# Performance work log

Hardware: AMD Instinct MI355X
Metric: run time of the kernel (lower is better)

## Reference

```python
import jax, jax.numpy as jnp
import numpy as np
from jax import lax

DIM = 128
DEPTH = 2
OUT_DIM = 256
DIM_HEAD = 64
HEADS = 8
WS = 16
INNER = DIM_HEAD * HEADS
EPS = 1e-5
SCALE = DIM_HEAD ** (-0.5)


def setup_inputs() -> dict:
    key = jax.random.key(0)
    ks = jax.random.split(key, 20)
    s = 0.02
    L = DEPTH
    inp = {
        "x": jax.random.normal(ks[0], (1, DIM, 256, 256), dtype=jnp.float32),
        "ln1_g": jnp.ones((L, DIM), dtype=jnp.float32),
        "ln1_b": jnp.zeros((L, DIM), dtype=jnp.float32),
        "wq": jax.random.normal(ks[1], (L, INNER, DIM), dtype=jnp.float32) * s,
        "wkv": jax.random.normal(ks[2], (L, 2 * INNER, DIM), dtype=jnp.float32) * s,
        "wo": jax.random.normal(ks[3], (L, DIM, INNER), dtype=jnp.float32) * s,
        "bo": jnp.zeros((L, DIM), dtype=jnp.float32),
        "ln2_g": jnp.ones((L, DIM), dtype=jnp.float32),
        "ln2_b": jnp.zeros((L, DIM), dtype=jnp.float32),
        "w_in": jax.random.normal(ks[4], (L, DIM, DIM), dtype=jnp.float32) * s,
        "b_in": jnp.zeros((L, DIM), dtype=jnp.float32),
        "w_c3": jax.random.normal(ks[5], (L, OUT_DIM, DIM, 3, 3), dtype=jnp.float32) * s,
        "b_c3": jnp.zeros((L, OUT_DIM), dtype=jnp.float32),
        "w_c1": jax.random.normal(ks[6], (L, DIM, OUT_DIM), dtype=jnp.float32) * s,
        "b_c1": jnp.zeros((L, DIM), dtype=jnp.float32),
        "w_outer": jax.random.normal(ks[7], (DIM, DIM), dtype=jnp.float32) * s,
        "b_outer": jnp.zeros((DIM,), dtype=jnp.float32),
    }
    return inp


def _layernorm(x, g, b):
    # channel-wise (dim=1) norm; note torch code uses (std + eps), not sqrt(var + eps)
    mean = jnp.mean(x, axis=1, keepdims=True)
    std = jnp.sqrt(jnp.var(x, axis=1, keepdims=True))
    return (x - mean) / (std + EPS) * g[None, :, None, None] + b[None, :, None, None]


def _conv1x1(w, x, b=None):
    y = jnp.einsum('oi,bihw->bohw', w, x)
    if b is not None:
        y = y + b[None, :, None, None]
    return y


def _to_windows(t, B, H, W):
    # [B, HEADS*DIM_HEAD, H, W] -> [B*HEADS*nx*ny, WS*WS, DIM_HEAD]
    nx, ny = H // WS, W // WS
    t = t.reshape(B, HEADS, DIM_HEAD, nx, WS, ny, WS)
    t = t.transpose(0, 1, 3, 5, 4, 6, 2)
    return t.reshape(B * HEADS * nx * ny, WS * WS, DIM_HEAD)


def _from_windows(t, B, H, W):
    nx, ny = H // WS, W // WS
    t = t.reshape(B, HEADS, nx, ny, WS, WS, DIM_HEAD)
    t = t.transpose(0, 1, 6, 2, 4, 3, 5)
    return t.reshape(B, HEADS * DIM_HEAD, H, W)


def _attention(x, wq_l, wkv_l, wo_l, bo_l):
    B, _, H, W = x.shape
    q = _conv1x1(wq_l, x)
    kv = _conv1x1(wkv_l, x)
    k, v = kv[:, :INNER], kv[:, INNER:]
    q = _to_windows(q, B, H, W)
    k = _to_windows(k, B, H, W)
    v = _to_windows(v, B, H, W)
    sim = jnp.einsum('bid,bjd->bij', q, k) * SCALE  # [nwin, 256, 256]
    attn = jax.nn.softmax(sim, axis=-1)
    out = jnp.einsum('bij,bjd->bid', attn, v)
    out = _from_windows(out, B, H, W)
    return _conv1x1(wo_l, out, bo_l)


def _feedforward(x, w_in_l, b_in_l, w_c3_l, b_c3_l, w_c1_l, b_c1_l):
    h = _conv1x1(w_in_l, x, b_in_l)
    h = lax.conv_general_dilated(h, w_c3_l, window_strides=(1, 1), padding='SAME',
                                 dimension_numbers=('NCHW', 'OIHW', 'NCHW'))
    h = h + b_c3_l[None, :, None, None]
    h = jax.nn.gelu(h, approximate=False)
    return _conv1x1(w_c1_l, h, b_c1_l)


def reference(x, ln1_g, ln1_b, wq, wkv, wo, bo, ln2_g, ln2_b,
              w_in, b_in, w_c3, b_c3, w_c1, b_c1, w_outer, b_outer):
    for l in range(DEPTH):
        xn = _layernorm(x, ln1_g[l], ln1_b[l])
        x = _attention(xn, wq[l], wkv[l], wo[l], bo[l]) + x
        xn = _layernorm(x, ln2_g[l], ln2_b[l])
        x = _feedforward(xn, w_in[l], b_in[l], w_c3[l], b_c3[l], w_c1[l], b_c1[l]) + x
    return _conv1x1(w_outer, x, b_outer) + x
```

## Files before the change

### kernel.cpp

```cpp
#include <hip/hip_runtime.h>
#include <hip/hip_bf16.h>
#include <math.h>

typedef __hip_bfloat16 bf16;
typedef float f4 __attribute__((ext_vector_type(4)));
typedef short s8 __attribute__((ext_vector_type(8)));
typedef unsigned int u2 __attribute__((ext_vector_type(2)));
typedef unsigned int u4v __attribute__((ext_vector_type(4)));

__device__ __forceinline__ void gload16(const void* g, char* l) {
  __builtin_amdgcn_global_load_lds(
      (const __attribute__((address_space(1))) unsigned int*)g,
      (__attribute__((address_space(3))) unsigned int*)l, 16, 0, 0);
}
__device__ __forceinline__ unsigned short bfr(float f) {
  bf16 h = __float2bfloat16(f);
  return *(unsigned short*)&h;
}
__device__ __forceinline__ unsigned int pk2(float a, float b) {
  return (unsigned int)bfr(a) | ((unsigned int)bfr(b) << 16);
}

__global__ __launch_bounds__(256) void prep_w(
    const float* __restrict__ wq, const float* __restrict__ wkv,
    const float* __restrict__ wo, const float* __restrict__ win,
    const float* __restrict__ wc3, const float* __restrict__ wc1,
    const float* __restrict__ wout, ushort* __restrict__ cw)
{
  int i = blockIdx.x * 256 + threadIdx.x;
  float v;
  if (i < 131072) v = wq[i];
  else if (i < 393216) v = wkv[i - 131072];
  else if (i < 524288) v = wo[i - 393216];
  else if (i < 557056) v = win[i - 524288];
  else if (i < 1146880) {
    int j = i - 557056; int lyr = j / 294912; int r = j - lyr * 294912;
    int m = r / 1152; int k = r - m * 1152; int tap = k >> 7; int ic = k & 127;
    v = wc3[(((size_t)lyr * 256 + m) * 128 + ic) * 9 + tap];
  }
  else if (i < 1212416) v = wc1[i - 1146880];
  else if (i < 1228800) v = wout[i - 1212416];
  else if (i < 1230848) { cw[i] = 0; return; }
  else return;
  cw[i] = bfr(v);
}

__global__ __launch_bounds__(256) void transpose_in(
    const float* __restrict__ x, float* __restrict__ xh)
{
  __shared__ float T[128][65];
  const int n0 = blockIdx.x * 64;
#pragma unroll
  for (int i = 0; i < 32; ++i) {
    int idx = i * 256 + threadIdx.x;
    int c = idx >> 6, nn = idx & 63;
    T[c][nn] = x[(size_t)c * 65536 + n0 + nn];
  }
  __syncthreads();
#pragma unroll
  for (int i = 0; i < 32; ++i) {
    int idx = i * 256 + threadIdx.x;
    int nn = idx >> 7, c = idx & 127;
    xh[(size_t)(n0 + nn) * 128 + c] = T[c][nn];
  }
}

__global__ __launch_bounds__(256) void ln_nhwc(
    const float* __restrict__ x, const float* __restrict__ g,
    const float* __restrict__ b, ushort* __restrict__ y)
{
  const int p = blockIdx.x * 256 + threadIdx.x;
  const f4* base = (const f4*)(x + (size_t)p * 128);
  f4 v[32];
  float s = 0.f, s2 = 0.f;
#pragma unroll
  for (int i = 0; i < 32; ++i) {
    v[i] = base[i];
#pragma unroll
    for (int j = 0; j < 4; ++j) { s += v[i][j]; s2 += v[i][j] * v[i][j]; }
  }
  float mean = s * (1.f / 128.f);
  float var = s2 * (1.f / 128.f) - mean * mean;
  var = var > 0.f ? var : 0.f;
  float inv = 1.f / (sqrtf(var) + 1e-5f);
  u2* dst = (u2*)(y + (size_t)p * 128);
#pragma unroll
  for (int i = 0; i < 32; ++i) {
    f4 gg = *(const f4*)(g + i * 4);
    f4 bb = *(const f4*)(b + i * 4);
    float f0 = (v[i][0] - mean) * inv * gg[0] + bb[0];
    float f1 = (v[i][1] - mean) * inv * gg[1] + bb[1];
    float f2 = (v[i][2] - mean) * inv * gg[2] + bb[2];
    float f3 = (v[i][3] - mean) * inv * gg[3] + bb[3];
    u2 st; st.x = pk2(f0, f1); st.y = pk2(f2, f3);
    dst[i] = st;
  }
}

__global__ __launch_bounds__(256) void to_bf16(
    const float* __restrict__ x, ushort* __restrict__ o)
{
  int i = blockIdx.x * 256 + threadIdx.x;
  f4 v = *(const f4*)(x + (size_t)i * 4);
  u2 st; st.x = pk2(v[0], v[1]); st.y = pk2(v[2], v[3]);
  *(u2*)(o + (size_t)i * 4) = st;
}

template<int MODE>
__global__ __launch_bounds__(256) void gemm_nhwc(
    const ushort* __restrict__ A, const ushort* __restrict__ X,
    const float* __restrict__ bias, const float* __restrict__ res,
    void* __restrict__ out, const int K, const int M)
{
  __shared__ __align__(16) char sm[32768];
  const int tid = threadIdx.x, w = tid >> 6, l = tid & 63;
  const int quad = l >> 4, l15 = l & 15;
  const int n0 = blockIdx.x * 128, m0 = blockIdx.y * 128;
  const int mh = (w & 1) * 64, nh = (w >> 1) * 64;
  const f4 fz = {0.f, 0.f, 0.f, 0.f};
  f4 acc[4][4];
#pragma unroll
  for (int a = 0; a < 4; ++a)
#pragma unroll
    for (int b2 = 0; b2 < 4; ++b2) acc[a][b2] = fz;

  const int KI = K >> 6;
  for (int kk = 0; kk < KI; ++kk) {
    if (kk) __syncthreads();
    const int k0 = kk << 6;
#pragma unroll
    for (int j = 0; j < 4; ++j) {
      int p = j * 256 + tid, r = p >> 3, c = (p & 7) ^ (r & 7);
      gload16(A + (size_t)(m0 + r) * K + k0 + c * 8, sm + (j * 256 + w * 64) * 16);
    }
#pragma unroll
    for (int j = 0; j < 4; ++j) {
      int p = j * 256 + tid, r = p >> 3, c = (p & 7) ^ (r & 7);
      gload16(X + (size_t)(n0 + r) * K + k0 + c * 8, sm + 16384 + (j * 256 + w * 64) * 16);
    }
    __syncthreads();
#pragma unroll
    for (int ks = 0; ks < 2; ++ks) {
      s8 af[4], bx[4];
#pragma unroll
      for (int mt = 0; mt < 4; ++mt) {
        int rr = mh + mt * 16 + l15;
        af[mt] = *(const s8*)(sm + rr * 128 + (((ks * 4 + quad) ^ (rr & 7)) << 4));
      }
#pragma unroll
      for (int nt = 0; nt < 4; ++nt) {
        int rr = nh + nt * 16 + l15;
        bx[nt] = *(const s8*)(sm + 16384 + rr * 128 + (((ks * 4 + quad) ^ (rr & 7)) << 4));
      }
#pragma unroll
      for (int mt = 0; mt < 4; ++mt)
#pragma unroll
        for (int nt = 0; nt < 4; ++nt)
          acc[mt][nt] = __builtin_amdgcn_mfma_f32_16x16x32_bf16(af[mt], bx[nt], acc[mt][nt], 0, 0, 0);
    }
  }
#pragma unroll
  for (int mt = 0; mt < 4; ++mt) {
#pragma unroll
    for (int nt = 0; nt < 4; ++nt) {
      const int m = m0 + mh + mt * 16 + quad * 4;
      const int n = n0 + nh + nt * 16 + l15;
      f4 bb = *(const f4*)(bias + m);
      f4 v = acc[mt][nt] + bb;
      if constexpr (MODE == 0) {
        u2 st; st.x = pk2(v[0], v[1]); st.y = pk2(v[2], v[3]);
        *(u2*)((ushort*)out + (size_t)n * M + m) = st;
      } else if constexpr (MODE == 1) {
        f4 r = *(const f4*)(res + (size_t)n * M + m);
        v += r;
        *(f4*)((float*)out + (size_t)n * M + m) = v;
      } else {
        f4 r = *(const f4*)(res + (size_t)n * M + m);
#pragma unroll
        for (int i = 0; i < 4; ++i)
          ((float*)out)[(size_t)(m + i) * 65536 + n] = v[i] + r[i];
      }
    }
  }
}

__global__ __launch_bounds__(256) void conv3_kernel(
    const ushort* __restrict__ A, const ushort* __restrict__ X,
    const float* __restrict__ bias, ushort* __restrict__ out,
    const ushort* __restrict__ zp)
{
  __shared__ __align__(16) char sm[32768];
  const int tid = threadIdx.x, w = tid >> 6, l = tid & 63;
  const int quad = l >> 4, l15 = l & 15;
  const int n0 = blockIdx.x * 128, m0 = blockIdx.y * 128;
  const int mh = (w & 1) * 64, nh = (w >> 1) * 64;
  const f4 fz = {0.f, 0.f, 0.f, 0.f};
  f4 acc[4][4];
#pragma unroll
  for (int a = 0; a < 4; ++a)
#pragma unroll
    for (int b2 = 0; b2 < 4; ++b2) acc[a][b2] = fz;

  for (int kk = 0; kk < 18; ++kk) {
    if (kk) __syncthreads();
    const int tap = kk >> 1, ky = tap / 3, kx = tap - ky * 3;
    const int dn = (ky - 1) * 256 + (kx - 1);
    const int kseg = (kk & 1) << 6;
#pragma unroll
    for (int j = 0; j < 4; ++j) {
      int p = j * 256 + tid, r = p >> 3, c = (p & 7) ^ (r & 7);
      gload16(A + (size_t)(m0 + r) * 1152 + kk * 64 + c * 8, sm + (j * 256 + w * 64) * 16);
    }
#pragma unroll
    for (int j = 0; j < 4; ++j) {
      int p = j * 256 + tid, r = p >> 3, c = (p & 7) ^ (r & 7);
      int nl = n0 + r;
      int ys = (nl >> 8) + ky - 1, xs = (nl & 255) + kx - 1;
      const ushort* gp = ((unsigned)ys < 256u && (unsigned)xs < 256u)
                         ? X + (size_t)(nl + dn) * 128 + kseg + c * 8 : zp;
      gload16(gp, sm + 16384 + (j * 256 + w * 64) * 16);
    }
    __syncthreads();
#pragma unroll
    for (int ks = 0; ks < 2; ++ks) {
      s8 af[4], bx[4];
#pragma unroll
      for (int mt = 0; mt < 4; ++mt) {
        int rr = mh + mt * 16 + l15;
        af[mt] = *(const s8*)(sm + rr * 128 + (((ks * 4 + quad) ^ (rr & 7)) << 4));
      }
#pragma unroll
      for (int nt = 0; nt < 4; ++nt) {
        int rr = nh + nt * 16 + l15;
        bx[nt] = *(const s8*)(sm + 16384 + rr * 128 + (((ks * 4 + quad) ^ (rr & 7)) << 4));
      }
#pragma unroll
      for (int mt = 0; mt < 4; ++mt)
#pragma unroll
        for (int nt = 0; nt < 4; ++nt)
          acc[mt][nt] = __builtin_amdgcn_mfma_f32_16x16x32_bf16(af[mt], bx[nt], acc[mt][nt], 0, 0, 0);
    }
  }
#pragma unroll
  for (int mt = 0; mt < 4; ++mt) {
#pragma unroll
    for (int nt = 0; nt < 4; ++nt) {
      const int m = m0 + mh + mt * 16 + quad * 4;
      const int n = n0 + nh + nt * 16 + l15;
      f4 bb = *(const f4*)(bias + m);
      f4 v = acc[mt][nt] + bb;
      float g0 = 0.5f * v[0] * (1.f + erff(v[0] * 0.70710678118f));
      float g1 = 0.5f * v[1] * (1.f + erff(v[1] * 0.70710678118f));
      float g2 = 0.5f * v[2] * (1.f + erff(v[2] * 0.70710678118f));
      float g3 = 0.5f * v[3] * (1.f + erff(v[3] * 0.70710678118f));
      u2 st; st.x = pk2(g0, g1); st.y = pk2(g2, g3);
      *(u2*)(out + (size_t)n * 256 + m) = st;
    }
  }
}

__global__ __launch_bounds__(256) void attn_kernel(
    const ushort* __restrict__ xn, const ushort* __restrict__ wq,
    const ushort* __restrict__ wkv, ushort* __restrict__ ao)
{
  __shared__ __align__(16) char sm[147456];
  const int tid = threadIdx.x, w = tid >> 6, l = tid & 63;
  const int quad = l >> 4, l15 = l & 15;
  const int win = blockIdx.x, head = blockIdx.y;
  const int nbase = ((win >> 4) << 12) + ((win & 15) << 4);
  char* RX = sm;
  char* RW = sm + 65536;
  char* RQ = sm + 81920;
  char* RK = sm + 114688;
  char* RVT = sm;
  char* RP = sm + 32768;
  const f4 fz = {0.f, 0.f, 0.f, 0.f};

#pragma unroll
  for (int j = 0; j < 16; ++j) {
    int p = j * 256 + tid, r = p >> 4, c = (p & 15) ^ (r & 15);
    int n = nbase + ((r >> 4) << 8) + (r & 15);
    gload16(xn + (size_t)n * 128 + c * 8, RX + (j * 256 + w * 64) * 16);
  }
  __syncthreads();

  f4 acc[4][4];
  for (int proj = 0; proj < 3; ++proj) {
    const ushort* wp = (proj == 0) ? wq + (size_t)head * 64 * 128
                     : (proj == 1) ? wkv + (size_t)head * 64 * 128
                                   : wkv + (size_t)(512 + head * 64) * 128;
#pragma unroll
    for (int j = 0; j < 4; ++j) {
      int p = j * 256 + tid, r = p >> 4, c = (p & 15) ^ (r & 15);
      gload16(wp + (size_t)r * 128 + c * 8, RW + (j * 256 + w * 64) * 16);
    }
    __syncthreads();
#pragma unroll
    for (int a = 0; a < 4; ++a)
#pragma unroll
      for (int b2 = 0; b2 < 4; ++b2) acc[a][b2] = fz;

    if (proj < 2) {
#pragma unroll
      for (int ks = 0; ks < 4; ++ks) {
        s8 af[4], bx[4];
#pragma unroll
        for (int mt = 0; mt < 4; ++mt) {
          int rr = mt * 16 + l15;
          af[mt] = *(const s8*)(RW + rr * 256 + (((ks * 4 + quad) ^ (rr & 15)) << 4));
        }
#pragma unroll
        for (int nt = 0; nt < 4; ++nt) {
          int rr = w * 64 + nt * 16 + l15;
          bx[nt] = *(const s8*)(RX + rr * 256 + (((ks * 4 + quad) ^ (rr & 15)) << 4));
        }
#pragma unroll
        for (int mt = 0; mt < 4; ++mt)
#pragma unroll
          for (int nt = 0; nt < 4; ++nt)
            acc[mt][nt] = __builtin_amdgcn_mfma_f32_16x16x32_bf16(af[mt], bx[nt], acc[mt][nt], 0, 0, 0);
      }
      char* RD = proj ? RK : RQ;
#pragma unroll
      for (int mt = 0; mt < 4; ++mt)
#pragma unroll
        for (int nt = 0; nt < 4; ++nt) {
          int tok = w * 64 + nt * 16 + l15, d0 = mt * 16 + quad * 4;
          char* a = RD + tok * 128 + (((d0 >> 3) ^ (tok & 7)) << 4) + (d0 & 7) * 2;
          *(unsigned int*)a = pk2(acc[mt][nt][0], acc[mt][nt][1]);
          *(unsigned int*)(a + 4) = pk2(acc[mt][nt][2], acc[mt][nt][3]);
        }
      __syncthreads();
    } else {
#pragma unroll
      for (int ks = 0; ks < 4; ++ks) {
        s8 af[4], bx[4];
#pragma unroll
        for (int mt = 0; mt < 4; ++mt) {
          int rr = w * 64 + mt * 16 + l15;
          af[mt] = *(const s8*)(RX + rr * 256 + (((ks * 4 + quad) ^ (rr & 15)) << 4));
        }
#pragma unroll
        for (int nt = 0; nt < 4; ++nt) {
          int rr = nt * 16 + l15;
          bx[nt] = *(const s8*)(RW + rr * 256 + (((ks * 4 + quad) ^ (rr & 15)) << 4));
        }
#pragma unroll
        for (int mt = 0; mt < 4; ++mt)
#pragma unroll
          for (int nt = 0; nt < 4; ++nt)
            acc[mt][nt] = __builtin_amdgcn_mfma_f32_16x16x32_bf16(af[mt], bx[nt], acc[mt][nt], 0, 0, 0);
      }
      __syncthreads();
#pragma unroll
      for (int mt = 0; mt < 4; ++mt)
#pragma unroll
        for (int nt = 0; nt < 4; ++nt) {
          int d = nt * 16 + l15, t0 = w * 64 + mt * 16 + quad * 4;
          char* a = RVT + d * 512 + (((t0 >> 3) ^ (d & 31)) << 4) + (t0 & 7) * 2;
          *(unsigned int*)a = pk2(acc[mt][nt][0], acc[mt][nt][1]);
          *(unsigned int*)(a + 4) = pk2(acc[mt][nt][2], acc[mt][nt][3]);
        }
      __syncthreads();
    }
  }

  f4 o[4][4];
  float lsum[4] = {0.f, 0.f, 0.f, 0.f};
#pragma unroll
  for (int a = 0; a < 4; ++a)
#pragma unroll
    for (int b2 = 0; b2 < 4; ++b2) o[a][b2] = fz;
  char* Pw = RP + w * 8192;

  for (int jt = 0; jt < 4; ++jt) {
    f4 s[4][4];
#pragma unroll
    for (int a = 0; a < 4; ++a)
#pragma unroll
      for (int b2 = 0; b2 < 4; ++b2) s[a][b2] = fz;
#pragma unroll
    for (int ks = 0; ks < 2; ++ks) {
      s8 af[4], bq[4];
#pragma unroll
      for (int mt = 0; mt < 4; ++mt) {
        int rr = jt * 64 + mt * 16 + l15;
        af[mt] = *(const s8*)(RK + rr * 128 + (((ks * 4 + quad) ^ (rr & 7)) << 4));
      }
#pragma unroll
      for (int nt = 0; nt < 4; ++nt) {
        int rr = w * 64 + nt * 16 + l15;
        bq[nt] = *(const s8*)(RQ + rr * 128 + (((ks * 4 + quad) ^ (rr & 7)) << 4));
      }
#pragma unroll
      for (int mt = 0; mt < 4; ++mt)
#pragma unroll
        for (int nt = 0; nt < 4; ++nt)
          s[mt][nt] = __builtin_amdgcn_mfma_f32_16x16x32_bf16(af[mt], bq[nt], s[mt][nt], 0, 0, 0);
    }
#pragma unroll
    for (int mt = 0; mt < 4; ++mt)
#pragma unroll
      for (int nt = 0; nt < 4; ++nt) {
        float p0 = __expf(s[mt][nt][0] * 0.125f);
        float p1 = __expf(s[mt][nt][1] * 0.125f);
        float p2 = __expf(s[mt][nt][2] * 0.125f);
        float p3 = __expf(s[mt][nt][3] * 0.125f);
        lsum[nt] += p0 + p1 + p2 + p3;
        int iL = nt * 16 + l15, j0 = mt * 16 + quad * 4;
        char* a = Pw + iL * 128 + (((j0 >> 3) ^ (iL & 7)) << 4) + (j0 & 7) * 2;
        *(unsigned int*)a = pk2(p0, p1);
        *(unsigned int*)(a + 4) = pk2(p2, p3);
      }
    __syncthreads();
#pragma unroll
    for (int ks = 0; ks < 2; ++ks) {
      s8 av[4], bp[4];
#pragma unroll
      for (int mt = 0; mt < 4; ++mt) {
        int d = mt * 16 + l15;
        av[mt] = *(const s8*)(RVT + d * 512 + (((jt * 8 + ks * 4 + quad) ^ (d & 31)) << 4));
      }
#pragma unroll
      for (int nt = 0; nt < 4; ++nt) {
        int iL = nt * 16 + l15;
        bp[nt] = *(const s8*)(Pw + iL * 128 + (((ks * 4 + quad) ^ (iL & 7)) << 4));
      }
#pragma unroll
      for (int mt = 0; mt < 4; ++mt)
#pragma unroll
        for (int nt = 0; nt < 4; ++nt)
          o[mt][nt] = __builtin_amdgcn_mfma_f32_16x16x32_bf16(av[mt], bp[nt], o[mt][nt], 0, 0, 0);
    }
    __syncthreads();
  }

  float inv[4];
#pragma unroll
  for (int nt = 0; nt < 4; ++nt) {
    float v = lsum[nt];
    v += __shfl_xor(v, 16, 64);
    v += __shfl_xor(v, 32, 64);
    inv[nt] = 1.f / v;
  }
#pragma unroll
  for (int mt = 0; mt < 4; ++mt)
#pragma unroll
    for (int nt = 0; nt < 4; ++nt) {
      int i = w * 64 + nt * 16 + l15, d0 = mt * 16 + quad * 4;
      char* a = RK + i * 128 + (((d0 >> 3) ^ (i & 7)) << 4) + (d0 & 7) * 2;
      *(unsigned int*)a = pk2(o[mt][nt][0] * inv[nt], o[mt][nt][1] * inv[nt]);
      *(unsigned int*)(a + 4) = pk2(o[mt][nt][2] * inv[nt], o[mt][nt][3] * inv[nt]);
    }
  __syncthreads();
  const int t = tid;
  const int n = nbase + ((t >> 4) << 8) + (t & 15);
  ushort* dst = ao + (size_t)n * 512 + head * 64;
#pragma unroll
  for (int c = 0; c < 8; ++c) {
    u4v v = *(const u4v*)(RK + t * 128 + ((c ^ (t & 7)) << 4));
    *(u4v*)(dst + c * 8) = v;
  }
}

extern "C" void kernel_launch(void* const* d_in, const int* in_sizes, int n_in,
                              void* d_out, int out_size, void* d_ws, size_t ws_size,
                              hipStream_t stream)
{
  const float* x_in    = (const float*)d_in[0];
  const float* ln1_g   = (const float*)d_in[1];
  const float* ln1_b   = (const float*)d_in[2];
  const float* wq      = (const float*)d_in[3];
  const float* wkv     = (const float*)d_in[4];
  const float* wo      = (const float*)d_in[5];
  const float* bo      = (const float*)d_in[6];
  const float* ln2_g   = (const float*)d_in[7];
  const float* ln2_b   = (const float*)d_in[8];
  const float* w_in    = (const float*)d_in[9];
  const float* b_in    = (const float*)d_in[10];
  const float* w_c3    = (const float*)d_in[11];
  const float* b_c3    = (const float*)d_in[12];
  const float* w_c1    = (const float*)d_in[13];
  const float* b_c1    = (const float*)d_in[14];
  const float* w_outer = (const float*)d_in[15];
  const float* b_outer = (const float*)d_in[16];

  char* wsb = (char*)d_ws;
  ushort* CW = (ushort*)wsb;
  float*  XH = (float*)(wsb + 4194304);
  ushort* XN = (ushort*)(wsb + 37748736);
  ushort* AO = (ushort*)(wsb + 54525952);
  ushort* H  = (ushort*)(wsb + 121634816);
  ushort* G  = (ushort*)(wsb + 138412032);
  ushort* XB = (ushort*)(wsb + 171966464);

  const ushort* zp = CW + 1228800;
  dim3 b256(256);

  prep_w<<<dim3(4808), b256, 0, stream>>>(wq, wkv, wo, w_in, w_c3, w_c1, w_outer, CW);
  transpose_in<<<dim3(1024), b256, 0, stream>>>(x_in, XH);

  for (int lyr = 0; lyr < 2; ++lyr) {
    const ushort* cwq = CW + lyr * 65536;
    const ushort* cwkv = CW + 131072 + lyr * 131072;
    const ushort* cwo = CW + 393216 + lyr * 65536;
    const ushort* cwin = CW + 524288 + lyr * 16384;
    const ushort* cw3 = CW + 557056 + lyr * 294912;
    const ushort* cwc1 = CW + 1146880 + lyr * 32768;

    ln_nhwc<<<dim3(256), b256, 0, stream>>>(XH, ln1_g + lyr * 128, ln1_b + lyr * 128, XN);
    attn_kernel<<<dim3(256, 8), b256, 0, stream>>>(XN, cwq, cwkv, AO);
    gemm_nhwc<1><<<dim3(512, 1), b256, 0, stream>>>(cwo, AO, bo + lyr * 128, XH, XH, 512, 128);
    ln_nhwc<<<dim3(256), b256, 0, stream>>>(XH, ln2_g + lyr * 128, ln2_b + lyr * 128, XN);
    gemm_nhwc<0><<<dim3(512, 1), b256, 0, stream>>>(cwin, XN, b_in + lyr * 128, nullptr, H, 128, 128);
    conv3_kernel<<<dim3(512, 2), b256, 0, stream>>>(cw3, H, b_c3 + lyr * 256, G, zp);
    gemm_nhwc<1><<<dim3(512, 1), b256, 0, stream>>>(cwc1, G, b_c1 + lyr * 128, XH, XH, 256, 128);
  }
  to_bf16<<<dim3(8192), b256, 0, stream>>>(XH, XB);
  gemm_nhwc<2><<<dim3(512, 1), b256, 0, stream>>>(CW + 1212416, XB, b_outer, XH, d_out, 128, 128);
}
```

Baseline: 696.7 us.

## Run window attention with 8 waves per block and drop inner-loop barriers

The attention kernel now launches 512 threads per window-head block, so each wave owns 32 query tokens instead of 64. The per-wave P buffer is private, which lets the two __syncthreads in the key-tile loop be removed. Accumulator tiles shrink, cutting register pressure to fit twice the waves. It also swaps the rounding bf16 pack for a truncating perm-based pack and uses exp2f with a prescaled constant; the truncation slightly lowers precision.

```diff
diff --git a/kernel.cpp b/kernel.cpp
--- a/kernel.cpp
+++ b/kernel.cpp
@@ -19,6 +19,9 @@
 }
 __device__ __forceinline__ unsigned int pk2(float a, float b) {
   return (unsigned int)bfr(a) | ((unsigned int)bfr(b) << 16);
+}
+__device__ __forceinline__ unsigned int pkt(float a, float b) {
+  return __builtin_amdgcn_perm(__float_as_uint(b), __float_as_uint(a), 0x07060302u);
 }
 
 __global__ __launch_bounds__(256) void prep_w(
@@ -259,7 +262,7 @@
   }
 }
 
-__global__ __launch_bounds__(256) void attn_kernel(
+__global__ __launch_bounds__(512) void attn_kernel(
     const ushort* __restrict__ xn, const ushort* __restrict__ wq,
     const ushort* __restrict__ wkv, ushort* __restrict__ ao)
 {
@@ -273,192 +276,233 @@
   char* RQ = sm + 81920;
   char* RK = sm + 114688;
   char* RVT = sm;
-  char* RP = sm + 32768;
+  char* Pw = sm + 32768 + w * 4096;
   const f4 fz = {0.f, 0.f, 0.f, 0.f};
 
 #pragma unroll
-  for (int j = 0; j < 16; ++j) {
-    int p = j * 256 + tid, r = p >> 4, c = (p & 15) ^ (r & 15);
+  for (int j = 0; j < 8; ++j) {
+    int p = j * 512 + tid, r = p >> 4, c = (p & 15) ^ (r & 15);
     int n = nbase + ((r >> 4) << 8) + (r & 15);
-    gload16(xn + (size_t)n * 128 + c * 8, RX + (j * 256 + w * 64) * 16);
-  }
-  __syncthreads();
-
-  f4 acc[4][4];
-  for (int proj = 0; proj < 3; ++proj) {
-    const ushort* wp = (proj == 0) ? wq + (size_t)head * 64 * 128
-                     : (proj == 1) ? wkv + (size_t)head * 64 * 128
-                                   : wkv + (size_t)(512 + head * 64) * 128;
-#pragma unroll
-    for (int j = 0; j < 4; ++j) {
-      int p = j * 256 + tid, r = p >> 4, c = (p & 15) ^ (r & 15);
-      gload16(wp + (size_t)r * 128 + c * 8, RW + (j * 256 + w * 64) * 16);
+    gload16(xn + (size_t)n * 128 + c * 8, RX + (j * 512 + w * 64) * 16);
+  }
+  const ushort* wpq = wq + (size_t)head * 64 * 128;
+#pragma unroll
+  for (int j = 0; j < 2; ++j) {
+    int p = j * 512 + tid, r = p >> 4, c = (p & 15) ^ (r & 15);
+    gload16(wpq + (size_t)r * 128 + c * 8, RW + (j * 512 + w * 64) * 16);
+  }
+  __syncthreads();
+
+  {
+    f4 acc[4][2];
+#pragma unroll
+    for (int a = 0; a < 4; ++a) { acc[a][0] = fz; acc[a][1] = fz; }
+#pragma unroll
+    for (int ks = 0; ks < 4; ++ks) {
+      s8 af[4], bx[2];
+#pragma unroll
+      for (int mt = 0; mt < 4; ++mt) {
+        int rr = mt * 16 + l15;
+        af[mt] = *(const s8*)(RW + rr * 256 + (((ks * 4 + quad) ^ (rr & 15)) << 4));
+      }
+#pragma unroll
+      for (int nt = 0; nt < 2; ++nt) {
+        int rr = w * 32 + nt * 16 + l15;
+        bx[nt] = *(const s8*)(RX + rr * 256 + (((ks * 4 + quad) ^ (rr & 15)) << 4));
+      }
+#pragma unroll
+      for (int mt = 0; mt < 4; ++mt)
+#pragma unroll
+        for (int nt = 0; nt < 2; ++nt)
+          acc[mt][nt] = __builtin_amdgcn_mfma_f32_16x16x32_bf16(af[mt], bx[nt], acc[mt][nt], 0, 0, 0);
+    }
+#pragma unroll
+    for (int mt = 0; mt < 4; ++mt)
+#pragma unroll
+      for (int nt = 0; nt < 2; ++nt) {
+        int tok = w * 32 + nt * 16 + l15, d0 = mt * 16 + quad * 4;
+        char* a = RQ + tok * 128 + (((d0 >> 3) ^ (tok & 7)) << 4) + (d0 & 7) * 2;
+        *(unsigned int*)a = pkt(acc[mt][nt][0], acc[mt][nt][1]);
+        *(unsigned int*)(a + 4) = pkt(acc[mt][nt][2], acc[mt][nt][3]);
+      }
+  }
+  __syncthreads();
+  const ushort* wpk = wkv + (size_t)head * 64 * 128;
+#pragma unroll
+  for (int j = 0; j < 2; ++j) {
+    int p = j * 512 + tid, r = p >> 4, c = (p & 15) ^ (r & 15);
+    gload16(wpk + (size_t)r * 128 + c * 8, RW + (j * 512 + w * 64) * 16);
+  }
+  __syncthreads();
+
+  {
+    f4 acc[4][2];
+#pragma unroll
+    for (int a = 0; a < 4; ++a) { acc[a][0] = fz; acc[a][1] = fz; }
+#pragma unroll
+    for (int ks = 0; ks < 4; ++ks) {
+      s8 af[4], bx[2];
+#pragma unroll
+      for (int mt = 0; mt < 4; ++mt) {
+        int rr = mt * 16 + l15;
+        af[mt] = *(const s8*)(RW + rr * 256 + (((ks * 4 + quad) ^ (rr & 15)) << 4));
+      }
+#pragma unroll
+      for (int nt = 0; nt < 2; ++nt) {
+        int rr = w * 32 + nt * 16 + l15;
+        bx[nt] = *(const s8*)(RX + rr * 256 + (((ks * 4 + quad) ^ (rr & 15)) << 4));
+      }
+#pragma unroll
+      for (int mt = 0; mt < 4; ++mt)
+#pragma unroll
+        for (int nt = 0; nt < 2; ++nt)
+          acc[mt][nt] = __builtin_amdgcn_mfma_f32_16x16x32_bf16(af[mt], bx[nt], acc[mt][nt], 0, 0, 0);
+    }
+#pragma unroll
+    for (int mt = 0; mt < 4; ++mt)
+#pragma unroll
+      for (int nt = 0; nt < 2; ++nt) {
+        int tok = w * 32 + nt * 16 + l15, d0 = mt * 16 + quad * 4;
+        char* a = RK + tok * 128 + (((d0 >> 3) ^ (tok & 7)) << 4) + (d0 & 7) * 2;
+        *(unsigned int*)a = pkt(acc[mt][nt][0], acc[mt][nt][1]);
+        *(unsigned int*)(a + 4) = pkt(acc[mt][nt][2], acc[mt][nt][3]);
+      }
+  }
+  __syncthreads();
+  const ushort* wpv = wkv + (size_t)(512 + head * 64) * 128;
+#pragma unroll
+  for (int j = 0; j < 2; ++j) {
+    int p = j * 512 + tid, r = p >> 4, c = (p & 15) ^ (r & 15);
+    gload16(wpv + (size_t)r * 128 + c * 8, RW + (j * 512 + w * 64) * 16);
+  }
+  __syncthreads();
+
+  {
+    f4 acc[2][4];
+#pragma unroll
+    for (int a = 0; a < 2; ++a)
+#pragma unroll
+      for (int b2 = 0; b2 < 4; ++b2) acc[a][b2] = fz;
+#pragma unroll
+    for (int ks = 0; ks < 4; ++ks) {
+      s8 ax[2], bw[4];
+#pragma unroll
+      for (int mt = 0; mt < 2; ++mt) {
+        int rr = w * 32 + mt * 16 + l15;
+        ax[mt] = *(const s8*)(RX + rr * 256 + (((ks * 4 + quad) ^ (rr & 15)) << 4));
+      }
+#pragma unroll
+      for (int nt = 0; nt < 4; ++nt) {
+        int rr = nt * 16 + l15;
+        bw[nt] = *(const s8*)(RW + rr * 256 + (((ks * 4 + quad) ^ (rr & 15)) << 4));
+      }
+#pragma unroll
+      for (int mt = 0; mt < 2; ++mt)
+#pragma unroll
+        for (int nt = 0; nt < 4; ++nt)
+          acc[mt][nt] = __builtin_amdgcn_mfma_f32_16x16x32_bf16(ax[mt], bw[nt], acc[mt][nt], 0, 0, 0);
     }
     __syncthreads();
 #pragma unroll
-    for (int a = 0; a < 4; ++a)
-#pragma unroll
-      for (int b2 = 0; b2 < 4; ++b2) acc[a][b2] = fz;
-
-    if (proj < 2) {
-#pragma unroll
-      for (int ks = 0; ks < 4; ++ks) {
-        s8 af[4], bx[4];
-#pragma unroll
-        for (int mt = 0; mt < 4; ++mt) {
-          int rr = mt * 16 + l15;
-          af[mt] = *(const s8*)(RW + rr * 256 + (((ks * 4 + quad) ^ (rr & 15)) << 4));
-        }
-#pragma unroll
-        for (int nt = 0; nt < 4; ++nt) {
-          int rr = w * 64 + nt * 16 + l15;
-          bx[nt] = *(const s8*)(RX + rr * 256 + (((ks * 4 + quad) ^ (rr & 15)) << 4));
-        }
-#pragma unroll
-        for (int mt = 0; mt < 4; ++mt)
-#pragma unroll
-          for (int nt = 0; nt < 4; ++nt)
-            acc[mt][nt] = __builtin_amdgcn_mfma_f32_16x16x32_bf16(af[mt], bx[nt], acc[mt][nt], 0, 0, 0);
-      }
-      char* RD = proj ? RK : RQ;
-#pragma unroll
-      for (int mt = 0; mt < 4; ++mt)
-#pragma unroll
-        for (int nt = 0; nt < 4; ++nt) {
-          int tok = w * 64 + nt * 16 + l15, d0 = mt * 16 + quad * 4;
-          char* a = RD + tok * 128 + (((d0 >> 3) ^ (tok & 7)) << 4) + (d0 & 7) * 2;
-          *(unsigned int*)a = pk2(acc[mt][nt][0], acc[mt][nt][1]);
-          *(unsigned int*)(a + 4) = pk2(acc[mt][nt][2], acc[mt][nt][3]);
-        }
-      __syncthreads();
-    } else {
-#pragma unroll
-      for (int ks = 0; ks < 4; ++ks) {
-        s8 af[4], bx[4];
-#pragma unroll
-        for (int mt = 0; mt < 4; ++mt) {
-          int rr = w * 64 + mt * 16 + l15;
-          af[mt] = *(const s8*)(RX + rr * 256 + (((ks * 4 + quad) ^ (rr & 15)) << 4));
-        }
-#pragma unroll
-        for (int nt = 0; nt < 4; ++nt) {
-          int rr = nt * 16 + l15;
-          bx[nt] = *(const s8*)(RW + rr * 256 + (((ks * 4 + quad) ^ (rr & 15)) << 4));
-        }
-#pragma unroll
-        for (int mt = 0; mt < 4; ++mt)
-#pragma unroll
-          for (int nt = 0; nt < 4; ++nt)
-            acc[mt][nt] = __builtin_amdgcn_mfma_f32_16x16x32_bf16(af[mt], bx[nt], acc[mt][nt], 0, 0, 0);
-      }
-      __syncthreads();
-#pragma unroll
-      for (int mt = 0; mt < 4; ++mt)
-#pragma unroll
-        for (int nt = 0; nt < 4; ++nt) {
-          int d = nt * 16 + l15, t0 = w * 64 + mt * 16 + quad * 4;
-          char* a = RVT + d * 512 + (((t0 >> 3) ^ (d & 31)) << 4) + (t0 & 7) * 2;
-          *(unsigned int*)a = pk2(acc[mt][nt][0], acc[mt][nt][1]);
-          *(unsigned int*)(a + 4) = pk2(acc[mt][nt][2], acc[mt][nt][3]);
-        }
-      __syncthreads();
-    }
-  }
-
-  f4 o[4][4];
-  float lsum[4] = {0.f, 0.f, 0.f, 0.f};
-#pragma unroll
-  for (int a = 0; a < 4; ++a)
-#pragma unroll
-    for (int b2 = 0; b2 < 4; ++b2) o[a][b2] = fz;
-  char* Pw = RP + w * 8192;
+    for (int mt = 0; mt < 2; ++mt)
+#pragma unroll
+      for (int nt = 0; nt < 4; ++nt) {
+        int d = nt * 16 + l15, t0 = w * 32 + mt * 16 + quad * 4;
+        char* a = RVT + d * 512 + (((t0 >> 3) ^ (d & 31)) << 4) + (t0 & 7) * 2;
+        *(unsigned int*)a = pkt(acc[mt][nt][0], acc[mt][nt][1]);
+        *(unsigned int*)(a + 4) = pkt(acc[mt][nt][2], acc[mt][nt][3]);
+      }
+  }
+  __syncthreads();
+
+  f4 o[4][2];
+  float lsum[2] = {0.f, 0.f};
+#pragma unroll
+  for (int a = 0; a < 4; ++a) { o[a][0] = fz; o[a][1] = fz; }
 
   for (int jt = 0; jt < 4; ++jt) {
-    f4 s[4][4];
-#pragma unroll
-    for (int a = 0; a < 4; ++a)
-#pragma unroll
-      for (int b2 = 0; b2 < 4; ++b2) s[a][b2] = fz;
+    f4 s[4][2];
+#pragma unroll
+    for (int a = 0; a < 4; ++a) { s[a][0] = fz; s[a][1] = fz; }
 #pragma unroll
     for (int ks = 0; ks < 2; ++ks) {
-      s8 af[4], bq[4];
+      s8 af[4], bq[2];
 #pragma unroll
       for (int mt = 0; mt < 4; ++mt) {
         int rr = jt * 64 + mt * 16 + l15;
         af[mt] = *(const s8*)(RK + rr * 128 + (((ks * 4 + quad) ^ (rr & 7)) << 4));
       }
 #pragma unroll
-      for (int nt = 0; nt < 4; ++nt) {
-        int rr = w * 64 + nt * 16 + l15;
+      for (int nt = 0; nt < 2; ++nt) {
+        int rr = w * 32 + nt * 16 + l15;
         bq[nt] = *(const s8*)(RQ + rr * 128 + (((ks * 4 + quad) ^ (rr & 7)) << 4));
       }
 #pragma unroll
       for (int mt = 0; mt < 4; ++mt)
 #pragma unroll
-        for (int nt = 0; nt < 4; ++nt)
+        for (int nt = 0; nt < 2; ++nt)
           s[mt][nt] = __builtin_amdgcn_mfma_f32_16x16x32_bf16(af[mt], bq[nt], s[mt][nt], 0, 0, 0);
     }
 #pragma unroll
     for (int mt = 0; mt < 4; ++mt)
 #pragma unroll
-      for (int nt = 0; nt < 4; ++nt) {
-        float p0 = __expf(s[mt][nt][0] * 0.125f);
-        float p1 = __expf(s[mt][nt][1] * 0.125f);
-        float p2 = __expf(s[mt][nt][2] * 0.125f);
-        float p3 = __expf(s[mt][nt][3] * 0.125f);
+      for (int nt = 0; nt < 2; ++nt) {
+        float p0 = exp2f(s[mt][nt][0] * 0.18033688f);
+        float p1 = exp2f(s[mt][nt][1] * 0.18033688f);
+        float p2 = exp2f(s[mt][nt][2] * 0.18033688f);
+        float p3 = exp2f(s[mt][nt][3] * 0.18033688f);
         lsum[nt] += p0 + p1 + p2 + p3;
         int iL = nt * 16 + l15, j0 = mt * 16 + quad * 4;
         char* a = Pw + iL * 128 + (((j0 >> 3) ^ (iL & 7)) << 4) + (j0 & 7) * 2;
-        *(unsigned int*)a = pk2(p0, p1);
-        *(unsigned int*)(a + 4) = pk2(p2, p3);
-      }
-    __syncthreads();
+        *(unsigned int*)a = pkt(p0, p1);
+        *(unsigned int*)(a + 4) = pkt(p2, p3);
+      }
 #pragma unroll
     for (int ks = 0; ks < 2; ++ks) {
-      s8 av[4], bp[4];
+      s8 av[4], bp[2];
 #pragma unroll
       for (int mt = 0; mt < 4; ++mt) {
         int d = mt * 16 + l15;
         av[mt] = *(const s8*)(RVT + d * 512 + (((jt * 8 + ks * 4 + quad) ^ (d & 31)) << 4));
       }
 #pragma unroll
-      for (int nt = 0; nt < 4; ++nt) {
+      for (int nt = 0; nt < 2; ++nt) {
         int iL = nt * 16 + l15;
         bp[nt] = *(const s8*)(Pw + iL * 128 + (((ks * 4 + quad) ^ (iL & 7)) << 4));
       }
 #pragma unroll
       for (int mt = 0; mt < 4; ++mt)
 #pragma unroll
-        for (int nt = 0; nt < 4; ++nt)
+        for (int nt = 0; nt < 2; ++nt)
           o[mt][nt] = __builtin_amdgcn_mfma_f32_16x16x32_bf16(av[mt], bp[nt], o[mt][nt], 0, 0, 0);
     }
-    __syncthreads();
-  }
-
-  float inv[4];
-#pragma unroll
-  for (int nt = 0; nt < 4; ++nt) {
+  }
+
+  float inv[2];
+#pragma unroll
+  for (int nt = 0; nt < 2; ++nt) {
     float v = lsum[nt];
     v += __shfl_xor(v, 16, 64);
     v += __shfl_xor(v, 32, 64);
     inv[nt] = 1.f / v;
   }
+  __syncthreads();
 #pragma unroll
   for (int mt = 0; mt < 4; ++mt)
 #pragma unroll
-    for (int nt = 0; nt < 4; ++nt) {
-      int i = w * 64 + nt * 16 + l15, d0 = mt * 16 + quad * 4;
-      char* a = RK + i * 128 + (((d0 >> 3) ^ (i & 7)) << 4) + (d0 & 7) * 2;
-      *(unsigned int*)a = pk2(o[mt][nt][0] * inv[nt], o[mt][nt][1] * inv[nt]);
-      *(unsigned int*)(a + 4) = pk2(o[mt][nt][2] * inv[nt], o[mt][nt][3] * inv[nt]);
-    }
-  __syncthreads();
-  const int t = tid;
-  const int n = nbase + ((t >> 4) << 8) + (t & 15);
-  ushort* dst = ao + (size_t)n * 512 + head * 64;
-#pragma unroll
-  for (int c = 0; c < 8; ++c) {
-    u4v v = *(const u4v*)(RK + t * 128 + ((c ^ (t & 7)) << 4));
+    for (int nt = 0; nt < 2; ++nt) {
+      int i = w * 32 + nt * 16 + l15, d0 = mt * 16 + quad * 4;
+      char* a = RQ + i * 128 + (((d0 >> 3) ^ (i & 7)) << 4) + (d0 & 7) * 2;
+      *(unsigned int*)a = pkt(o[mt][nt][0] * inv[nt], o[mt][nt][1] * inv[nt]);
+      *(unsigned int*)(a + 4) = pkt(o[mt][nt][2] * inv[nt], o[mt][nt][3] * inv[nt]);
+    }
+  __syncthreads();
+  const int tok = tid >> 1, half = tid & 1;
+  const int n = nbase + ((tok >> 4) << 8) + (tok & 15);
+  ushort* dst = ao + (size_t)n * 512 + head * 64 + half * 32;
+#pragma unroll
+  for (int c = 0; c < 4; ++c) {
+    u4v v = *(const u4v*)(RQ + tok * 128 + (((half * 4 + c) ^ (tok & 7)) << 4));
     *(u4v*)(dst + c * 8) = v;
   }
 }
@@ -509,7 +553,7 @@
     const ushort* cwc1 = CW + 1146880 + lyr * 32768;
 
     ln_nhwc<<<dim3(256), b256, 0, stream>>>(XH, ln1_g + lyr * 128, ln1_b + lyr * 128, XN);
-    attn_kernel<<<dim3(256, 8), b256, 0, stream>>>(XN, cwq, cwkv, AO);
+    attn_kernel<<<dim3(256, 8), dim3(512), 0, stream>>>(XN, cwq, cwkv, AO);
     gemm_nhwc<1><<<dim3(512, 1), b256, 0, stream>>>(cwo, AO, bo + lyr * 128, XH, XH, 512, 128);
     ln_nhwc<<<dim3(256), b256, 0, stream>>>(XH, ln2_g + lyr * 128, ln2_b + lyr * 128, XN);
     gemm_nhwc<0><<<dim3(512, 1), b256, 0, stream>>>(cwin, XN, b_in + lyr * 128, nullptr, H, 128, 128);
```

New measurement: 666.5 us. -4.3%, faster.
